# Optimization experiments

Hardware: AMD Instinct MI355X
Metric: run time of the kernel (lower is better)

## Reference

```python
import jax, jax.numpy as jnp
import numpy as np

EPS = 1e-5
NEG_SLOPE = 0.01


def setup_inputs() -> dict:
    key = jax.random.key(0)
    ks = jax.random.split(key, 5)
    B, T, I, H = 16, 16384, 64, 128
    s = 1.0 / np.sqrt(H)
    return {
        "x": jax.random.normal(ks[0], (B, T, I), dtype=jnp.float32),
        "W_ih": jax.random.normal(ks[1], (4 * H, I), dtype=jnp.float32) * s,
        "W_hh": jax.random.normal(ks[2], (4 * H, H), dtype=jnp.float32) * s,
        "b_ih": jax.random.normal(ks[3], (4 * H,), dtype=jnp.float32) * s,
        "b_hh": jax.random.normal(ks[4], (4 * H,), dtype=jnp.float32) * s,
        "gamma": jnp.ones((H,), dtype=jnp.float32),
        "beta": jnp.zeros((H,), dtype=jnp.float32),
    }


def _lstm(x, W_ih, W_hh, b_ih, b_hh):
    B, T, _ = x.shape
    H = W_hh.shape[1]
    # Precompute input contributions for all timesteps: [B, T, 4H]
    gx = jnp.einsum('bti,gi->btg', x, W_ih) + b_ih + b_hh

    def step(carry, g_t):
        h, c = carry
        g = g_t + h @ W_hh.T  # [B, 4H]
        i, f, gg, o = jnp.split(g, 4, axis=-1)  # PyTorch gate order i,f,g,o
        i = jax.nn.sigmoid(i)
        f = jax.nn.sigmoid(f)
        gg = jnp.tanh(gg)
        o = jax.nn.sigmoid(o)
        c = f * c + i * gg
        h = o * jnp.tanh(c)
        return (h, c), h

    h0 = jnp.zeros((B, H), dtype=x.dtype)
    (hn, cn), out = jax.lax.scan(step, (h0, h0), jnp.swapaxes(gx, 0, 1))
    return jnp.swapaxes(out, 0, 1), hn, cn  # out: [B, T, H]


def reference(x, W_ih, W_hh, b_ih, b_hh, gamma, beta):
    B, T, _ = x.shape
    H = W_hh.shape[1]
    out, hn, cn = _lstm(x, W_ih, W_hh, b_ih, b_hh)
    # BatchNorm1d (training mode) over flattened [B*T, H]
    flat = out.reshape(-1, H)
    mean = flat.mean(axis=0)
    var = flat.var(axis=0)  # biased variance, as PyTorch uses for normalization
    norm = (flat - mean) * jax.lax.rsqrt(var + EPS) * gamma + beta
    y = jax.nn.leaky_relu(norm.reshape(B, T, H), NEG_SLOPE)
    return (y, (hn[None], cn[None]))  # hn/cn: [num_layers=1, B, H]
```

## Files before the change

### kernel.cpp

```cpp
#include <hip/hip_runtime.h>
#include <hip/hip_bf16.h>
#include <cstdint>

#define TB 16
#define TT 16384
#define TI 64
#define TH 128
#define TG 512

typedef _Float16 f16x8 __attribute__((ext_vector_type(8)));
typedef float    f32x4 __attribute__((ext_vector_type(4)));

typedef const float __attribute__((address_space(1)))* gcfp;
typedef float __attribute__((address_space(1)))*       gfp;

__device__ __forceinline__ float sigf(float z) {
    return 1.0f / (1.0f + __expf(-z));
}
__device__ __forceinline__ float tanhf_fast(float z) {
    return 2.0f / (1.0f + __expf(-2.0f * z)) - 1.0f;
}
__device__ __forceinline__ float4 ld4(const float* p) {
    return *reinterpret_cast<const float4*>(p);
}
__device__ __forceinline__ void fma4(float4& acc, const float4 w, const float4 h) {
    acc.x = fmaf(w.x, h.x, acc.x);
    acc.y = fmaf(w.y, h.y, acc.y);
    acc.z = fmaf(w.z, h.z, acc.z);
    acc.w = fmaf(w.w, h.w, acc.w);
}
__device__ __forceinline__ float hsum4(const float4 a) {
    return (a.x + a.y) + (a.z + a.w);
}
__device__ __forceinline__ void pin_agpr(f16x8& v) {
    asm volatile("" : "+a"(v));
}

__global__ __launch_bounds__(256, 2) void gx_precompute(
    const float* __restrict__ x, const float* __restrict__ W_ih,
    const float* __restrict__ b_ih, const float* __restrict__ b_hh,
    float* __restrict__ gx)
{
    const int tid  = threadIdx.x;
    const int j    = tid & (TH - 1);
    const int pair = tid >> 7;
    const int row_a = pair * 2 * TH + j;
    const int row_b = row_a + TH;

    float4 ua[TI / 4], ub[TI / 4];
#pragma unroll
    for (int k4 = 0; k4 < TI / 4; ++k4) {
        ua[k4] = ld4(W_ih + (size_t)row_a * TI + k4 * 4);
        ub[k4] = ld4(W_ih + (size_t)row_b * TI + k4 * 4);
    }
    const float bias_a = b_ih[row_a] + b_hh[row_a];
    const float bias_b = b_ih[row_b] + b_hh[row_b];

    __shared__ __align__(16) float xs[2][TI];
    const int ROWS = 128;
    const size_t r0 = (size_t)blockIdx.x * ROWS;

    if (tid < TI / 4)
        *reinterpret_cast<float4*>(&xs[0][tid * 4]) = ld4(x + r0 * TI + tid * 4);
    __syncthreads();
    float4 xreg = make_float4(0.f, 0.f, 0.f, 0.f);
    if (tid < TI / 4) xreg = ld4(x + (r0 + 1) * TI + tid * 4);

#pragma unroll 1
    for (int rr = 0; rr < ROWS; ++rr) {
        const float* xrow = xs[rr & 1];
        float4 aa = make_float4(0.f, 0.f, 0.f, 0.f);
        float4 ab = make_float4(0.f, 0.f, 0.f, 0.f);
#pragma unroll
        for (int k4 = 0; k4 < TI / 4; ++k4) {
            const float4 x4 = *reinterpret_cast<const float4*>(&xrow[k4 * 4]);
            fma4(aa, ua[k4], x4);
            fma4(ab, ub[k4], x4);
        }
        if (tid < TI / 4) {
            if (rr + 1 < ROWS)
                *reinterpret_cast<float4*>(&xs[(rr + 1) & 1][tid * 4]) = xreg;
            if (rr + 2 < ROWS) xreg = ld4(x + (r0 + rr + 2) * TI + tid * 4);
        }
        float* grow = gx + (r0 + rr) * (size_t)TG;
        grow[row_a] = hsum4(aa) + bias_a;
        grow[row_b] = hsum4(ab) + bias_b;

        asm volatile("s_waitcnt lgkmcnt(0)" ::: "memory");
        __builtin_amdgcn_s_barrier();
    }
}

__global__
__attribute__((amdgpu_flat_work_group_size(512, 512), amdgpu_waves_per_eu(2, 2)))
void lstm_scan_mfma(
    const float* __restrict__ W_hh, const float* __restrict__ gx,
    float* __restrict__ y, float* __restrict__ hn, float* __restrict__ cn)
{
    const int b    = blockIdx.x;
    const int tid  = threadIdx.x;
    const int w    = tid >> 6;
    const int lane = tid & 63;
    const int c    = lane & 15;
    const int oct  = lane >> 4;

    __shared__ __align__(16) _Float16 h_lds[2][TH];

    f16x8 bf[4][4];
#pragma unroll
    for (int s = 0; s < 4; ++s) {
#pragma unroll
        for (int kt = 0; kt < 4; ++kt) {
            const float* wr =
                W_hh + (size_t)(s * TH + 16 * w + c) * TH + kt * 32 + oct * 8;
            const float4 lo = ld4(wr);
            const float4 hi = ld4(wr + 4);
            bf[s][kt] = f16x8{(_Float16)lo.x, (_Float16)lo.y, (_Float16)lo.z,
                              (_Float16)lo.w, (_Float16)hi.x, (_Float16)hi.y,
                              (_Float16)hi.z, (_Float16)hi.w};
        }
    }
#pragma unroll
    for (int s = 0; s < 4; ++s)
#pragma unroll
        for (int kt = 0; kt < 4; ++kt) pin_agpr(bf[s][kt]);

    if (tid < TH) h_lds[0][tid] = (_Float16)0.f;

    float c_state = 0.0f;
    float h_keep  = 0.0f;

    gcfp gxp = (gcfp)(gx + (size_t)b * TT * TG + 16 * w + c);
    float gr[4][4];
#pragma unroll
    for (int sl = 0; sl < 4; ++sl) {
#pragma unroll
        for (int s = 0; s < 4; ++s)
            gr[sl][s] = gxp[(size_t)sl * TG + s * TH];
    }
    gxp += 4 * (size_t)TG;

    gfp yp = (gfp)(y + (size_t)b * TT * TH + 16 * w + c);

    __syncthreads();

    const f32x4 kz = {0.f, 0.f, 0.f, 0.f};

#define STEP(SLOT, CUR, NXT)                                                   \
    {                                                                          \
                  \
        f16x8 a0 = *(const f16x8*)&h_lds[CUR][0 * 32 + oct * 8];               \
        f16x8 a1 = *(const f16x8*)&h_lds[CUR][1 * 32 + oct * 8];               \
        f16x8 a2 = *(const f16x8*)&h_lds[CUR][2 * 32 + oct * 8];               \
        f16x8 a3 = *(const f16x8*)&h_lds[CUR][3 * 32 + oct * 8];               \
        f32x4 q0 = __builtin_amdgcn_mfma_f32_16x16x32_f16(a0, bf[0][0], kz, 0, 0, 0); \
        f32x4 q1 = __builtin_amdgcn_mfma_f32_16x16x32_f16(a0, bf[1][0], kz, 0, 0, 0); \
        f32x4 q2 = __builtin_amdgcn_mfma_f32_16x16x32_f16(a0, bf[2][0], kz, 0, 0, 0); \
        f32x4 q3 = __builtin_amdgcn_mfma_f32_16x16x32_f16(a0, bf[3][0], kz, 0, 0, 0); \
        q0 = __builtin_amdgcn_mfma_f32_16x16x32_f16(a1, bf[0][1], q0, 0, 0, 0);\
        q1 = __builtin_amdgcn_mfma_f32_16x16x32_f16(a1, bf[1][1], q1, 0, 0, 0);\
        q2 = __builtin_amdgcn_mfma_f32_16x16x32_f16(a1, bf[2][1], q2, 0, 0, 0);\
        q3 = __builtin_amdgcn_mfma_f32_16x16x32_f16(a1, bf[3][1], q3, 0, 0, 0);\
        q0 = __builtin_amdgcn_mfma_f32_16x16x32_f16(a2, bf[0][2], q0, 0, 0, 0);\
        q1 = __builtin_amdgcn_mfma_f32_16x16x32_f16(a2, bf[1][2], q1, 0, 0, 0);\
        q2 = __builtin_amdgcn_mfma_f32_16x16x32_f16(a2, bf[2][2], q2, 0, 0, 0);\
        q3 = __builtin_amdgcn_mfma_f32_16x16x32_f16(a2, bf[3][2], q3, 0, 0, 0);\
        q0 = __builtin_amdgcn_mfma_f32_16x16x32_f16(a3, bf[0][3], q0, 0, 0, 0);\
        q1 = __builtin_amdgcn_mfma_f32_16x16x32_f16(a3, bf[1][3], q1, 0, 0, 0);\
        q2 = __builtin_amdgcn_mfma_f32_16x16x32_f16(a3, bf[2][3], q2, 0, 0, 0);\
        q3 = __builtin_amdgcn_mfma_f32_16x16x32_f16(a3, bf[3][3], q3, 0, 0, 0);\
        const float p0 = q0[0] + gr[SLOT][0];                                  \
        const float p1 = q1[0] + gr[SLOT][1];                                  \
        const float p2 = q2[0] + gr[SLOT][2];                                  \
        const float p3 = q3[0] + gr[SLOT][3];                                  \
                     \
        gr[SLOT][0] = gxp[0 * TH];                                             \
        gr[SLOT][1] = gxp[1 * TH];                                             \
        gr[SLOT][2] = gxp[2 * TH];                                             \
        gr[SLOT][3] = gxp[3 * TH];                                             \
        gxp += TG;                                                             \
        const float gi = sigf(p0);                                             \
        const float gf = sigf(p1);                                             \
        const float gg = tanhf_fast(p2);                                       \
        const float go = sigf(p3);                                             \
        c_state = fmaf(gf, c_state, gi * gg);                                  \
        h_keep  = go * tanhf_fast(c_state);                                    \
        if (lane < 16) {                                                       \
            h_lds[NXT][16 * w + c] = (_Float16)h_keep;                         \
            *yp = h_keep;                                                      \
        }                                                                      \
        yp += TH;                                                              \
        asm volatile("s_waitcnt lgkmcnt(0)" ::: "memory");                     \
        __builtin_amdgcn_s_barrier();                                          \
    }

#pragma unroll 1
    for (int t = 0; t < TT; t += 4) {
        STEP(0, 0, 1)
        STEP(1, 1, 0)
        STEP(2, 0, 1)
        STEP(3, 1, 0)
    }
#undef STEP

    if (lane < 16) {
        ((gfp)(hn))[(size_t)b * TH + 16 * w + c] = h_keep;
        ((gfp)(cn))[(size_t)b * TH + 16 * w + c] = c_state;
    }
}

__global__ __launch_bounds__(512, 2) void lstm_scan_fused(
    const float* __restrict__ x, const float* __restrict__ W_ih,
    const float* __restrict__ W_hh, const float* __restrict__ b_ih,
    const float* __restrict__ b_hh,
    float* __restrict__ y, float* __restrict__ hn, float* __restrict__ cn)
{
    const int b    = blockIdx.x;
    const int tid  = threadIdx.x;
    const int j    = tid & (TH - 1);
    const int gate = tid >> 7;

    __shared__ __align__(16) float h_lds[TH];
    __shared__ __align__(16) float g_lds[TG];
    __shared__ __align__(16) float xs[2][TI];

    float4 w[TH / 4];
#pragma unroll
    for (int k4 = 0; k4 < TH / 4; ++k4)
        w[k4] = ld4(W_hh + (size_t)tid * TH + k4 * 4);
    float4 u[TI / 4];
#pragma unroll
    for (int k4 = 0; k4 < TI / 4; ++k4)
        u[k4] = ld4(W_ih + (size_t)tid * TI + k4 * 4);
    const float bias = b_ih[tid] + b_hh[tid];

    if (tid < TH) h_lds[tid] = 0.0f;
    float c_state = 0.0f;
    float h_keep  = 0.0f;

    float4 xreg = make_float4(0.f, 0.f, 0.f, 0.f);
    const float* xp = x + ((size_t)b * TT + 2) * TI;
    float* yp = y + (size_t)b * TT * TH;

    if (tid < TI / 4)
        *reinterpret_cast<float4*>(&xs[0][tid * 4]) =
            ld4(x + ((size_t)b * TT + 0) * TI + tid * 4);
    __syncthreads();
    if (tid < TI / 4)
        xreg = ld4(x + ((size_t)b * TT + 1) * TI + tid * 4);

#pragma unroll 1
    for (int t = 0; t < TT; ++t) {
        float4 acc = make_float4(0.f, 0.f, 0.f, 0.f);
#pragma unroll
        for (int k4 = 0; k4 < TH / 4; ++k4) {
            const float4 h4 = *reinterpret_cast<const float4*>(&h_lds[k4 * 4]);
            fma4(acc, w[k4], h4);
        }
        float p = hsum4(acc);
        {
            float4 fx = make_float4(0.f, 0.f, 0.f, 0.f);
            const float* xrow = xs[t & 1];
#pragma unroll
            for (int k4 = 0; k4 < TI / 4; ++k4) {
                const float4 x4 = *reinterpret_cast<const float4*>(&xrow[k4 * 4]);
                fma4(fx, u[k4], x4);
            }
            p += hsum4(fx) + bias;
        }

        const float act = (gate == 2) ? tanhf_fast(p) : sigf(p);
        g_lds[tid] = act;

        asm volatile("s_waitcnt lgkmcnt(0)" ::: "memory");
        __builtin_amdgcn_s_barrier();

        if (tid < TH) {
            const float gi = g_lds[j];
            const float gf = g_lds[TH + j];
            const float gg = g_lds[2 * TH + j];
            const float go = g_lds[3 * TH + j];
            c_state = fmaf(gf, c_state, gi * gg);
            h_keep  = go * tanhf_fast(c_state);
            h_lds[j] = h_keep;
            yp[(size_t)t * TH + j] = h_keep;
        }

        if (tid < TI / 4) {
            if (t + 1 < TT)
                *reinterpret_cast<float4*>(&xs[(t + 1) & 1][tid * 4]) = xreg;
            if (t + 2 < TT) xreg = ld4(xp + tid * 4);
        }
        xp += TI;

        asm volatile("s_waitcnt lgkmcnt(0)" ::: "memory");
        __builtin_amdgcn_s_barrier();
    }

    if (tid < TH) {
        hn[(size_t)b * TH + j] = h_keep;
        cn[(size_t)b * TH + j] = c_state;
    }
}

__global__ void bn_zero(float* ws) { ws[threadIdx.x] = 0.0f; }

__global__ __launch_bounds__(256) void bn_stats(const float* __restrict__ y,
                                                float* __restrict__ ws)
{
    const int tid  = threadIdx.x;
    const int col4 = tid & 31;
    const int rg   = tid >> 5;
    const int NROW = TB * TT;
    float4 s = make_float4(0.f, 0.f, 0.f, 0.f);
    float4 q = make_float4(0.f, 0.f, 0.f, 0.f);
    for (int row = blockIdx.x * 8 + rg; row < NROW; row += gridDim.x * 8) {
        const float4 v = ld4(y + (size_t)row * TH + col4 * 4);
        s.x += v.x; s.y += v.y; s.z += v.z; s.w += v.w;
        q.x = fmaf(v.x, v.x, q.x); q.y = fmaf(v.y, v.y, q.y);
        q.z = fmaf(v.z, v.z, q.z); q.w = fmaf(v.w, v.w, q.w);
    }
    __shared__ float4 ls[256], lq[256];
    ls[tid] = s; lq[tid] = q;
    __syncthreads();
    if (tid < 32) {
        float4 S = ls[tid], Q = lq[tid];
        for (int g2 = 1; g2 < 8; ++g2) {
            const float4 a = ls[g2 * 32 + tid], b2 = lq[g2 * 32 + tid];
            S.x += a.x; S.y += a.y; S.z += a.z; S.w += a.w;
            Q.x += b2.x; Q.y += b2.y; Q.z += b2.z; Q.w += b2.w;
        }
        atomicAdd(&ws[tid * 4 + 0], S.x); atomicAdd(&ws[tid * 4 + 1], S.y);
        atomicAdd(&ws[tid * 4 + 2], S.z); atomicAdd(&ws[tid * 4 + 3], S.w);
        atomicAdd(&ws[TH + tid * 4 + 0], Q.x); atomicAdd(&ws[TH + tid * 4 + 1], Q.y);
        atomicAdd(&ws[TH + tid * 4 + 2], Q.z); atomicAdd(&ws[TH + tid * 4 + 3], Q.w);
    }
}

__global__ __launch_bounds__(256) void bn_apply(float* __restrict__ y,
                                                const float* __restrict__ ws,
                                                const float* __restrict__ gamma,
                                                const float* __restrict__ beta)
{
    const int tid  = threadIdx.x;
    const int col4 = tid & 31;
    const int rg   = tid >> 5;
    const int NROW = TB * TT;
    const float invN = 1.0f / (float)(TB * TT);

    const float4 sm = ld4(ws + col4 * 4);
    const float4 sq = ld4(ws + TH + col4 * 4);
    const float4 gm = ld4(gamma + col4 * 4);
    const float4 bt = ld4(beta + col4 * 4);
    float4 mean, scale, shift;
    mean.x = sm.x * invN; mean.y = sm.y * invN;
    mean.z = sm.z * invN; mean.w = sm.w * invN;
    scale.x = rsqrtf(fmaf(-mean.x, mean.x, sq.x * invN) + 1e-5f) * gm.x;
    scale.y = rsqrtf(fmaf(-mean.y, mean.y, sq.y * invN) + 1e-5f) * gm.y;
    scale.z = rsqrtf(fmaf(-mean.z, mean.z, sq.z * invN) + 1e-5f) * gm.z;
    scale.w = rsqrtf(fmaf(-mean.w, mean.w, sq.w * invN) + 1e-5f) * gm.w;
    shift.x = bt.x - mean.x * scale.x; shift.y = bt.y - mean.y * scale.y;
    shift.z = bt.z - mean.z * scale.z; shift.w = bt.w - mean.w * scale.w;

    for (int row = blockIdx.x * 8 + rg; row < NROW; row += gridDim.x * 8) {
        float* p = y + (size_t)row * TH + col4 * 4;
        float4 v = *reinterpret_cast<const float4*>(p);
        v.x = fmaf(v.x, scale.x, shift.x); v.y = fmaf(v.y, scale.y, shift.y);
        v.z = fmaf(v.z, scale.z, shift.z); v.w = fmaf(v.w, scale.w, shift.w);
        v.x = fmaxf(v.x, 0.01f * v.x); v.y = fmaxf(v.y, 0.01f * v.y);
        v.z = fmaxf(v.z, 0.01f * v.z); v.w = fmaxf(v.w, 0.01f * v.w);
        *reinterpret_cast<float4*>(p) = v;
    }
}

extern "C" void kernel_launch(void* const* d_in, const int* in_sizes, int n_in,
                              void* d_out, int out_size, void* d_ws, size_t ws_size,
                              hipStream_t stream)
{
    const float* x     = (const float*)d_in[0];
    const float* W_ih  = (const float*)d_in[1];
    const float* W_hh  = (const float*)d_in[2];
    const float* b_ih  = (const float*)d_in[3];
    const float* b_hh  = (const float*)d_in[4];
    const float* gamma = (const float*)d_in[5];
    const float* beta  = (const float*)d_in[6];

    float* y  = (float*)d_out;
    float* hn = y + (size_t)TB * TT * TH;
    float* cn = hn + TB * TH;

    float* ws_stats = (float*)d_ws;
    const size_t GX_BYTES = (size_t)TB * TT * TG * sizeof(float);
    const bool use_ws = ws_size >= GX_BYTES + 4096 + 4 * TG * sizeof(float);

    bn_zero<<<1, 256, 0, stream>>>(ws_stats);

    if (use_ws) {
        float* gxbuf = (float*)((char*)d_ws + 4096);
        gx_precompute<<<2048, 256, 0, stream>>>(x, W_ih, b_ih, b_hh, gxbuf);
        lstm_scan_mfma<<<TB, 512, 0, stream>>>(W_hh, gxbuf, y, hn, cn);
    } else {
        lstm_scan_fused<<<TB, 512, 0, stream>>>(x, W_ih, W_hh, b_ih, b_hh,
                                                y, hn, cn);
    }

    bn_stats<<<512, 256, 0, stream>>>(y, ws_stats);
    bn_apply<<<2048, 256, 0, stream>>>(y, ws_stats, gamma, beta);
}
```

Measured before the change: 10.49 ms.

## Split LSTM scan into four compute waves plus a gx producer wave

The recurrent scan kernel now uses five waves instead of eight. Four compute waves each own 32 hidden channels and hold twice as many f16 W_hh fragments pinned in AGPRs. A fifth wave streams the precomputed gx rows into double-buffered LDS one step ahead, so compute waves no longer issue global loads on the serial path. The aim is to cut barrier participants and per-step global-load latency, at the cost of twice the MFMA work per compute wave and extra LDS traffic for gx.

```diff
diff --git a/kernel.cpp b/kernel.cpp
--- a/kernel.cpp
+++ b/kernel.cpp
@@ -92,8 +92,8 @@
 }
 
 __global__
-__attribute__((amdgpu_flat_work_group_size(512, 512), amdgpu_waves_per_eu(2, 2)))
-void lstm_scan_mfma(
+__attribute__((amdgpu_flat_work_group_size(320, 320), amdgpu_waves_per_eu(1, 2)))
+void lstm_scan_mfma5(
     const float* __restrict__ W_hh, const float* __restrict__ gx,
     float* __restrict__ y, float* __restrict__ hn, float* __restrict__ cn)
 {
@@ -103,90 +103,101 @@
     const int lane = tid & 63;
     const int c    = lane & 15;
     const int oct  = lane >> 4;
+    const int uu   = oct & 1;
+    const int ch   = 32 * (w & 3) + 16 * uu + c;
 
     __shared__ __align__(16) _Float16 h_lds[2][TH];
-
-    f16x8 bf[4][4];
-#pragma unroll
-    for (int s = 0; s < 4; ++s) {
-#pragma unroll
-        for (int kt = 0; kt < 4; ++kt) {
-            const float* wr =
-                W_hh + (size_t)(s * TH + 16 * w + c) * TH + kt * 32 + oct * 8;
-            const float4 lo = ld4(wr);
-            const float4 hi = ld4(wr + 4);
-            bf[s][kt] = f16x8{(_Float16)lo.x, (_Float16)lo.y, (_Float16)lo.z,
-                              (_Float16)lo.w, (_Float16)hi.x, (_Float16)hi.y,
-                              (_Float16)hi.z, (_Float16)hi.w};
-        }
-    }
-#pragma unroll
-    for (int s = 0; s < 4; ++s)
-#pragma unroll
-        for (int kt = 0; kt < 4; ++kt) pin_agpr(bf[s][kt]);
-
-    if (tid < TH) h_lds[0][tid] = (_Float16)0.f;
+    __shared__ __align__(16) float    gx_lds[2][TG];
 
     float c_state = 0.0f;
     float h_keep  = 0.0f;
 
-    gcfp gxp = (gcfp)(gx + (size_t)b * TT * TG + 16 * w + c);
-    float gr[4][4];
-#pragma unroll
-    for (int sl = 0; sl < 4; ++sl) {
+    f16x8 bf[4][2][4];
+    float4 va, vb;
+    const float4* g4 = reinterpret_cast<const float4*>(gx + (size_t)b * TT * TG);
+
+    if (w < 4) {
+#pragma unroll
+        for (int s = 0; s < 4; ++s) {
+#pragma unroll
+            for (int u = 0; u < 2; ++u) {
+#pragma unroll
+                for (int kt = 0; kt < 4; ++kt) {
+                    const float* wr = W_hh +
+                        (size_t)(s * TH + 32 * w + 16 * u + c) * TH + kt * 32 + oct * 8;
+                    const float4 lo = ld4(wr);
+                    const float4 hi = ld4(wr + 4);
+                    bf[s][u][kt] = f16x8{(_Float16)lo.x, (_Float16)lo.y,
+                                         (_Float16)lo.z, (_Float16)lo.w,
+                                         (_Float16)hi.x, (_Float16)hi.y,
+                                         (_Float16)hi.z, (_Float16)hi.w};
+                }
+            }
+        }
 #pragma unroll
         for (int s = 0; s < 4; ++s)
-            gr[sl][s] = gxp[(size_t)sl * TG + s * TH];
-    }
-    gxp += 4 * (size_t)TG;
-
-    gfp yp = (gfp)(y + (size_t)b * TT * TH + 16 * w + c);
-
-    __syncthreads();
+#pragma unroll
+            for (int u = 0; u < 2; ++u)
+#pragma unroll
+                for (int kt = 0; kt < 4; ++kt) pin_agpr(bf[s][u][kt]);
+
+        if (tid < TH) h_lds[0][tid] = (_Float16)0.f;
+    } else {
+        va = g4[lane];
+        vb = g4[lane + 64];
+        *reinterpret_cast<float4*>(&gx_lds[0][lane * 4])       = va;
+        *reinterpret_cast<float4*>(&gx_lds[0][256 + lane * 4]) = vb;
+        va = g4[128 + lane];
+        vb = g4[128 + lane + 64];
+        g4 += 256;
+    }
+
+    asm volatile("s_waitcnt lgkmcnt(0)" ::: "memory");
+    __builtin_amdgcn_s_barrier();
 
     const f32x4 kz = {0.f, 0.f, 0.f, 0.f};
 
-#define STEP(SLOT, CUR, NXT)                                                   \
+    if (w < 4) {
+        gfp yp = (gfp)(y + (size_t)b * TT * TH + ch);
+
+#define CSTEP(S)                                                               \
     {                                                                          \
-                  \
-        f16x8 a0 = *(const f16x8*)&h_lds[CUR][0 * 32 + oct * 8];               \
-        f16x8 a1 = *(const f16x8*)&h_lds[CUR][1 * 32 + oct * 8];               \
-        f16x8 a2 = *(const f16x8*)&h_lds[CUR][2 * 32 + oct * 8];               \
-        f16x8 a3 = *(const f16x8*)&h_lds[CUR][3 * 32 + oct * 8];               \
-        f32x4 q0 = __builtin_amdgcn_mfma_f32_16x16x32_f16(a0, bf[0][0], kz, 0, 0, 0); \
-        f32x4 q1 = __builtin_amdgcn_mfma_f32_16x16x32_f16(a0, bf[1][0], kz, 0, 0, 0); \
-        f32x4 q2 = __builtin_amdgcn_mfma_f32_16x16x32_f16(a0, bf[2][0], kz, 0, 0, 0); \
-        f32x4 q3 = __builtin_amdgcn_mfma_f32_16x16x32_f16(a0, bf[3][0], kz, 0, 0, 0); \
-        q0 = __builtin_amdgcn_mfma_f32_16x16x32_f16(a1, bf[0][1], q0, 0, 0, 0);\
-        q1 = __builtin_amdgcn_mfma_f32_16x16x32_f16(a1, bf[1][1], q1, 0, 0, 0);\
-        q2 = __builtin_amdgcn_mfma_f32_16x16x32_f16(a1, bf[2][1], q2, 0, 0, 0);\
-        q3 = __builtin_amdgcn_mfma_f32_16x16x32_f16(a1, bf[3][1], q3, 0, 0, 0);\
-        q0 = __builtin_amdgcn_mfma_f32_16x16x32_f16(a2, bf[0][2], q0, 0, 0, 0);\
-        q1 = __builtin_amdgcn_mfma_f32_16x16x32_f16(a2, bf[1][2], q1, 0, 0, 0);\
-        q2 = __builtin_amdgcn_mfma_f32_16x16x32_f16(a2, bf[2][2], q2, 0, 0, 0);\
-        q3 = __builtin_amdgcn_mfma_f32_16x16x32_f16(a2, bf[3][2], q3, 0, 0, 0);\
-        q0 = __builtin_amdgcn_mfma_f32_16x16x32_f16(a3, bf[0][3], q0, 0, 0, 0);\
-        q1 = __builtin_amdgcn_mfma_f32_16x16x32_f16(a3, bf[1][3], q1, 0, 0, 0);\
-        q2 = __builtin_amdgcn_mfma_f32_16x16x32_f16(a3, bf[2][3], q2, 0, 0, 0);\
-        q3 = __builtin_amdgcn_mfma_f32_16x16x32_f16(a3, bf[3][3], q3, 0, 0, 0);\
-        const float p0 = q0[0] + gr[SLOT][0];                                  \
-        const float p1 = q1[0] + gr[SLOT][1];                                  \
-        const float p2 = q2[0] + gr[SLOT][2];                                  \
-        const float p3 = q3[0] + gr[SLOT][3];                                  \
-                     \
-        gr[SLOT][0] = gxp[0 * TH];                                             \
-        gr[SLOT][1] = gxp[1 * TH];                                             \
-        gr[SLOT][2] = gxp[2 * TH];                                             \
-        gr[SLOT][3] = gxp[3 * TH];                                             \
-        gxp += TG;                                                             \
+        f16x8 a0 = *(const f16x8*)&h_lds[S][0 * 32 + oct * 8];                 \
+        f16x8 a1 = *(const f16x8*)&h_lds[S][1 * 32 + oct * 8];                 \
+        f16x8 a2 = *(const f16x8*)&h_lds[S][2 * 32 + oct * 8];                 \
+        f16x8 a3 = *(const f16x8*)&h_lds[S][3 * 32 + oct * 8];                 \
+        const float g0 = gx_lds[S][0 * TH + ch];                               \
+        const float g1 = gx_lds[S][1 * TH + ch];                               \
+        const float g2 = gx_lds[S][2 * TH + ch];                               \
+        const float g3 = gx_lds[S][3 * TH + ch];                               \
+        float pv[4][2];                                                        \
+        _Pragma("unroll")                                                      \
+        for (int s = 0; s < 4; ++s) {                                          \
+            _Pragma("unroll")                                                  \
+            for (int u = 0; u < 2; ++u) {                                      \
+                f32x4 qa = __builtin_amdgcn_mfma_f32_16x16x32_f16(             \
+                    a0, bf[s][u][0], kz, 0, 0, 0);                             \
+                qa = __builtin_amdgcn_mfma_f32_16x16x32_f16(                   \
+                    a1, bf[s][u][1], qa, 0, 0, 0);                             \
+                f32x4 qb = __builtin_amdgcn_mfma_f32_16x16x32_f16(             \
+                    a2, bf[s][u][2], kz, 0, 0, 0);                             \
+                qb = __builtin_amdgcn_mfma_f32_16x16x32_f16(                   \
+                    a3, bf[s][u][3], qb, 0, 0, 0);                             \
+                pv[s][u] = qa[0] + qb[0];                                      \
+            }                                                                  \
+        }                                                                      \
+        const float p0 = (uu ? pv[0][1] : pv[0][0]) + g0;                      \
+        const float p1 = (uu ? pv[1][1] : pv[1][0]) + g1;                      \
+        const float p2 = (uu ? pv[2][1] : pv[2][0]) + g2;                      \
+        const float p3 = (uu ? pv[3][1] : pv[3][0]) + g3;                      \
         const float gi = sigf(p0);                                             \
         const float gf = sigf(p1);                                             \
         const float gg = tanhf_fast(p2);                                       \
         const float go = sigf(p3);                                             \
         c_state = fmaf(gf, c_state, gi * gg);                                  \
         h_keep  = go * tanhf_fast(c_state);                                    \
-        if (lane < 16) {                                                       \
-            h_lds[NXT][16 * w + c] = (_Float16)h_keep;                         \
+        if (lane < 32) {                                                       \
+            h_lds[S ^ 1][ch] = (_Float16)h_keep;                               \
             *yp = h_keep;                                                      \
         }                                                                      \
         yp += TH;                                                              \
@@ -195,17 +206,35 @@
     }
 
 #pragma unroll 1
-    for (int t = 0; t < TT; t += 4) {
-        STEP(0, 0, 1)
-        STEP(1, 1, 0)
-        STEP(2, 0, 1)
-        STEP(3, 1, 0)
-    }
-#undef STEP
-
-    if (lane < 16) {
-        ((gfp)(hn))[(size_t)b * TH + 16 * w + c] = h_keep;
-        ((gfp)(cn))[(size_t)b * TH + 16 * w + c] = c_state;
+        for (int t = 0; t < TT; t += 2) {
+            CSTEP(0)
+            CSTEP(1)
+        }
+#undef CSTEP
+
+        if (lane < 32) {
+            ((gfp)(hn))[(size_t)b * TH + ch] = h_keep;
+            ((gfp)(cn))[(size_t)b * TH + ch] = c_state;
+        }
+    } else {
+#define PSTEP(S)                                                               \
+    {                                                                          \
+                    \
+        *reinterpret_cast<float4*>(&gx_lds[S ^ 1][lane * 4])       = va;       \
+        *reinterpret_cast<float4*>(&gx_lds[S ^ 1][256 + lane * 4]) = vb;       \
+        va = g4[lane];                                                         \
+        vb = g4[lane + 64];                                                    \
+        g4 += 128;                                                             \
+        asm volatile("s_waitcnt lgkmcnt(0)" ::: "memory");                     \
+        __builtin_amdgcn_s_barrier();                                          \
+    }
+
+#pragma unroll 1
+        for (int t = 0; t < TT; t += 2) {
+            PSTEP(0)
+            PSTEP(1)
+        }
+#undef PSTEP
     }
 }
 
@@ -398,7 +427,7 @@
     if (use_ws) {
         float* gxbuf = (float*)((char*)d_ws + 4096);
         gx_precompute<<<2048, 256, 0, stream>>>(x, W_ih, b_ih, b_hh, gxbuf);
-        lstm_scan_mfma<<<TB, 512, 0, stream>>>(W_hh, gxbuf, y, hn, cn);
+        lstm_scan_mfma5<<<TB, 320, 0, stream>>>(W_hh, gxbuf, y, hn, cn);
     } else {
         lstm_scan_fused<<<TB, 512, 0, stream>>>(x, W_ih, W_hh, b_ih, b_hh,
                                                 y, hn, cn);
```

Measured after the change: 9.048 ms (median of 2 runs). -13.8%, faster.
